# Kernel optimization log

Measured on AMD Instinct MI355X. Metric: run time of the kernel, lower is better.

The kernel has to match this reference:

```python
import jax, jax.numpy as jnp
import numpy as np

N_NODES = 50000
N_EDGES = 600000
N_GRAPHS = 64
D_IN = 128
D_HID = 128
D_OUT = 64


def setup_inputs() -> dict:
    key = jax.random.key(0)
    ks = jax.random.split(key, 8)
    x = jax.random.normal(ks[0], (N_NODES, D_IN), dtype=jnp.float32)
    edge_index = jax.random.randint(ks[1], (2, N_EDGES), 0, N_NODES, dtype=jnp.int64)
    batch = jnp.sort(jax.random.randint(ks[2], (N_NODES,), 0, N_GRAPHS, dtype=jnp.int64))
    def glorot(k, fan_in, fan_out):
        s = jnp.sqrt(6.0 / (fan_in + fan_out))
        return jax.random.uniform(k, (fan_in, fan_out), jnp.float32, -s, s)
    return {
        "x": x, "edge_index": edge_index, "batch": batch,
        "W1": glorot(ks[3], D_IN, D_HID), "b1": jnp.zeros((D_HID,), jnp.float32),
        "W2": glorot(ks[4], D_HID, D_HID), "b2": jnp.zeros((D_HID,), jnp.float32),
        "W3": glorot(ks[5], D_HID, D_HID), "b3": jnp.zeros((D_HID,), jnp.float32),
        "W4": glorot(ks[6], D_HID, D_OUT), "b4": jnp.zeros((D_OUT,), jnp.float32),
    }


def _gcn_conv(x, W, b, src, dst, deg_inv_sqrt, n_nodes):
    # PyG GCNConv: h = x W; out_i = sum_{j->i} norm_ij h_j  (+ self loop) + b
    h = x @ W  # [N, F]
    norm = deg_inv_sqrt[src] * deg_inv_sqrt[dst]  # [E]
    agg = jax.ops.segment_sum(h[src] * norm[:, None], dst, num_segments=n_nodes)
    # self-loop contribution: norm_ii = deg_inv_sqrt[i]^2
    agg = agg + h * (deg_inv_sqrt * deg_inv_sqrt)[:, None]
    return agg + b


def reference(x, edge_index, batch, W1, b1, W2, b2, W3, b3, W4, b4):
    n = x.shape[0]
    src, dst = edge_index[0], edge_index[1]
    # degree including self loops (PyG add_self_loops + deg over dst)
    deg = jax.ops.segment_sum(jnp.ones_like(dst, dtype=x.dtype), dst, num_segments=n) + 1.0
    deg_inv_sqrt = jax.lax.rsqrt(deg)

    h = jax.nn.relu(_gcn_conv(x, W1, b1, src, dst, deg_inv_sqrt, n))
    h = jax.nn.relu(_gcn_conv(h, W2, b2, src, dst, deg_inv_sqrt, n))
    h = jax.nn.relu(_gcn_conv(h, W3, b3, src, dst, deg_inv_sqrt, n))
    h = _gcn_conv(h, W4, b4, src, dst, deg_inv_sqrt, n)

    # global mean pool over graphs in the batch
    sums = jax.ops.segment_sum(h, batch, num_segments=N_GRAPHS)  # [G, D_OUT]
    cnts = jax.ops.segment_sum(jnp.ones((n,), h.dtype), batch, num_segments=N_GRAPHS)
    hg = sums / jnp.maximum(cnts, 1.0)[:, None]
    return jnp.squeeze(hg)
```

## Files before the change

kernel.cpp:

```cpp
#include <hip/hip_runtime.h>
#include <hip/hip_bf16.h>

#define N_NODES 50000
#define N_EDGES 600000
#define N_GRAPHS 64
#define PCHUNK 16

typedef __attribute__((ext_vector_type(8))) short bf16x8;
typedef __attribute__((ext_vector_type(4))) float f32x4;

__device__ __forceinline__ unsigned short f2bf(float f) {
    unsigned int u = __float_as_uint(f);
    unsigned int r = u + 0x7fffu + ((u >> 16) & 1u);
    return (unsigned short)(r >> 16);
}
__device__ __forceinline__ float bf_lo(unsigned int u) { return __uint_as_float(u << 16); }
__device__ __forceinline__ float bf_hi(unsigned int u) { return __uint_as_float(u & 0xffff0000u); }
__device__ __forceinline__ float bf1(unsigned short s) {
    return __uint_as_float((unsigned int)s << 16);
}

__device__ __forceinline__ void wprep_one(const float* W, unsigned short* Wp, int F, int idx) {
    int i = idx & 7;
    int lane = (idx >> 3) & 63;
    int ks = (idx >> 9) & 3;
    int ct = idx >> 11;
    int k = ks * 32 + (lane >> 4) * 8 + i;
    int col = ct * 16 + (lane & 15);
    Wp[idx] = f2bf(W[(size_t)k * F + col]);
}

__global__ __launch_bounds__(256) void deg_wprep(const int* __restrict__ dst,
                                                 int* __restrict__ degi, int E,
                                                 const float* __restrict__ W1,
                                                 const float* __restrict__ W2,
                                                 const float* __restrict__ W3,
                                                 const float* __restrict__ W4,
                                                 unsigned short* __restrict__ Wp1,
                                                 unsigned short* __restrict__ Wp2,
                                                 unsigned short* __restrict__ Wp3,
                                                 unsigned short* __restrict__ Wp4) {
    const int DEGB = (N_EDGES + 255) / 256;
    int bid = blockIdx.x;
    if (bid < DEGB) {
        int i = bid * 256 + threadIdx.x;
        if (i < E) atomicAdd(&degi[dst[i]], 1);
    } else {
        int wb = bid - DEGB;
        if (wb < 64) wprep_one(W1, Wp1, 128, wb * 256 + threadIdx.x);
        else if (wb < 128) wprep_one(W2, Wp2, 128, (wb - 64) * 256 + threadIdx.x);
        else if (wb < 192) wprep_one(W3, Wp3, 128, (wb - 128) * 256 + threadIdx.x);
        else wprep_one(W4, Wp4, 64, (wb - 192) * 256 + threadIdx.x);
    }
}

__global__ __launch_bounds__(256) void scan_block(const int* __restrict__ in,
                                                  int* __restrict__ excl,
                                                  int* __restrict__ bsum,
                                                  float* __restrict__ dis, int N) {
    __shared__ int s[256];
    int i = blockIdx.x * 256 + threadIdx.x;
    int v = (i < N) ? in[i] : 0;
    s[threadIdx.x] = v;
    __syncthreads();
#pragma unroll
    for (int off = 1; off < 256; off <<= 1) {
        int t = (threadIdx.x >= off) ? s[threadIdx.x - off] : 0;
        __syncthreads();
        s[threadIdx.x] += t;
        __syncthreads();
    }
    if (i < N) {
        excl[i] = s[threadIdx.x] - v;
        dis[i] = rsqrtf((float)v + 1.0f);
    }
    if (threadIdx.x == 255) bsum[blockIdx.x] = s[255];
}

__global__ __launch_bounds__(256) void scan_top(const int* __restrict__ bsum,
                                                int* __restrict__ boff, int NB,
                                                const int* __restrict__ batch,
                                                int* __restrict__ gstart, int N) {
    __shared__ int s[256];
    int v = (threadIdx.x < NB) ? bsum[threadIdx.x] : 0;
    s[threadIdx.x] = v;
    __syncthreads();
#pragma unroll
    for (int off = 1; off < 256; off <<= 1) {
        int t = (threadIdx.x >= off) ? s[threadIdx.x - off] : 0;
        __syncthreads();
        s[threadIdx.x] += t;
        __syncthreads();
    }
    if (threadIdx.x < NB) boff[threadIdx.x] = s[threadIdx.x] - v;

    int g = threadIdx.x;
    if (g <= N_GRAPHS) {
        int lo = 0, hi = N;
        while (lo < hi) {
            int mid = (lo + hi) >> 1;
            if (batch[mid] < g) lo = mid + 1; else hi = mid;
        }
        gstart[g] = lo;
    }
}

__global__ __launch_bounds__(256) void scan_fix(const int* __restrict__ excl,
                                                const int* __restrict__ boff,
                                                int* __restrict__ rowptr,
                                                int* __restrict__ cursor, int N, int E) {
    int i = blockIdx.x * 256 + threadIdx.x;
    if (i < N) {
        int r = excl[i] + boff[blockIdx.x];
        rowptr[i] = r;
        cursor[i] = r;
    }
    if (i == 0) rowptr[N] = E;
}

__global__ __launch_bounds__(256) void csr_fill(const int* __restrict__ src,
                                                const int* __restrict__ dst,
                                                const float* __restrict__ dis,
                                                int* __restrict__ cursor,
                                                int2* __restrict__ csr, int E) {
    int e = blockIdx.x * blockDim.x + threadIdx.x;
    if (e >= E) return;
    int s = src[e];
    int d = dst[e];
    float nrm = dis[s] * dis[d];
    int pos = atomicAdd(&cursor[d], 1);
    csr[pos] = make_int2(s, __float_as_int(nrm));
}

__device__ __forceinline__ void gather128(int beg, int end, const int2* __restrict__ csr,
                                          const unsigned short* __restrict__ T, int lane,
                                          float& ax, float& ay) {
    int p = beg;
    for (; p + 8 <= end; p += 8) {
        int2 e0 = csr[p], e1 = csr[p + 1], e2 = csr[p + 2], e3 = csr[p + 3];
        int2 e4 = csr[p + 4], e5 = csr[p + 5], e6 = csr[p + 6], e7 = csr[p + 7];
        unsigned int r0 = *reinterpret_cast<const unsigned int*>(T + (size_t)e0.x * 128 + lane * 2);
        unsigned int r1 = *reinterpret_cast<const unsigned int*>(T + (size_t)e1.x * 128 + lane * 2);
        unsigned int r2 = *reinterpret_cast<const unsigned int*>(T + (size_t)e2.x * 128 + lane * 2);
        unsigned int r3 = *reinterpret_cast<const unsigned int*>(T + (size_t)e3.x * 128 + lane * 2);
        unsigned int r4 = *reinterpret_cast<const unsigned int*>(T + (size_t)e4.x * 128 + lane * 2);
        unsigned int r5 = *reinterpret_cast<const unsigned int*>(T + (size_t)e5.x * 128 + lane * 2);
        unsigned int r6 = *reinterpret_cast<const unsigned int*>(T + (size_t)e6.x * 128 + lane * 2);
        unsigned int r7 = *reinterpret_cast<const unsigned int*>(T + (size_t)e7.x * 128 + lane * 2);
        float n0 = __int_as_float(e0.y), n1 = __int_as_float(e1.y);
        float n2 = __int_as_float(e2.y), n3 = __int_as_float(e3.y);
        float n4 = __int_as_float(e4.y), n5 = __int_as_float(e5.y);
        float n6 = __int_as_float(e6.y), n7 = __int_as_float(e7.y);
        ax = fmaf(n0, bf_lo(r0), ax); ay = fmaf(n0, bf_hi(r0), ay);
        ax = fmaf(n1, bf_lo(r1), ax); ay = fmaf(n1, bf_hi(r1), ay);
        ax = fmaf(n2, bf_lo(r2), ax); ay = fmaf(n2, bf_hi(r2), ay);
        ax = fmaf(n3, bf_lo(r3), ax); ay = fmaf(n3, bf_hi(r3), ay);
        ax = fmaf(n4, bf_lo(r4), ax); ay = fmaf(n4, bf_hi(r4), ay);
        ax = fmaf(n5, bf_lo(r5), ax); ay = fmaf(n5, bf_hi(r5), ay);
        ax = fmaf(n6, bf_lo(r6), ax); ay = fmaf(n6, bf_hi(r6), ay);
        ax = fmaf(n7, bf_lo(r7), ax); ay = fmaf(n7, bf_hi(r7), ay);
    }
    for (; p + 4 <= end; p += 4) {
        int2 e0 = csr[p], e1 = csr[p + 1], e2 = csr[p + 2], e3 = csr[p + 3];
        unsigned int r0 = *reinterpret_cast<const unsigned int*>(T + (size_t)e0.x * 128 + lane * 2);
        unsigned int r1 = *reinterpret_cast<const unsigned int*>(T + (size_t)e1.x * 128 + lane * 2);
        unsigned int r2 = *reinterpret_cast<const unsigned int*>(T + (size_t)e2.x * 128 + lane * 2);
        unsigned int r3 = *reinterpret_cast<const unsigned int*>(T + (size_t)e3.x * 128 + lane * 2);
        float n0 = __int_as_float(e0.y), n1 = __int_as_float(e1.y);
        float n2 = __int_as_float(e2.y), n3 = __int_as_float(e3.y);
        ax = fmaf(n0, bf_lo(r0), ax); ay = fmaf(n0, bf_hi(r0), ay);
        ax = fmaf(n1, bf_lo(r1), ax); ay = fmaf(n1, bf_hi(r1), ay);
        ax = fmaf(n2, bf_lo(r2), ax); ay = fmaf(n2, bf_hi(r2), ay);
        ax = fmaf(n3, bf_lo(r3), ax); ay = fmaf(n3, bf_hi(r3), ay);
    }
    for (; p < end; ++p) {
        int2 ed = csr[p];
        float nrm = __int_as_float(ed.y);
        unsigned int r = *reinterpret_cast<const unsigned int*>(T + (size_t)ed.x * 128 + lane * 2);
        ax = fmaf(nrm, bf_lo(r), ax);
        ay = fmaf(nrm, bf_hi(r), ay);
    }
}

__global__ __launch_bounds__(256) void mm_mfma1(const float* __restrict__ Xf,
                                                const unsigned short* __restrict__ Wp,
                                                unsigned short* __restrict__ T, int N) {
    const int lane = threadIdx.x & 63;
    const int wave = threadIdx.x >> 6;
    const int r0 = blockIdx.x * 64 + wave * 16;
    const int kg = lane >> 4;
    const int rdrow = min(r0 + (lane & 15), N - 1);
    const float* xr = Xf + (size_t)rdrow * 128;

    bf16x8 a[4];
#pragma unroll
    for (int ks = 0; ks < 4; ++ks) {
        const int kb = ks * 32 + kg * 8;
        float4 x0 = *reinterpret_cast<const float4*>(xr + kb);
        float4 x1 = *reinterpret_cast<const float4*>(xr + kb + 4);
        float v[8] = {x0.x, x0.y, x0.z, x0.w, x1.x, x1.y, x1.z, x1.w};
#pragma unroll
        for (int i = 0; i < 8; ++i) a[ks][i] = (short)f2bf(v[i]);
    }

#pragma unroll
    for (int ct = 0; ct < 8; ++ct) {
        f32x4 acc = {0.f, 0.f, 0.f, 0.f};
#pragma unroll
        for (int ks = 0; ks < 4; ++ks) {
            bf16x8 b = *reinterpret_cast<const bf16x8*>(Wp + ((size_t)(ct * 4 + ks) * 64 + lane) * 8);
            acc = __builtin_amdgcn_mfma_f32_16x16x32_bf16(a[ks], b, acc, 0, 0, 0);
        }
        const int col = ct * 16 + (lane & 15);
#pragma unroll
        for (int r = 0; r < 4; ++r) {
            const int rowm = r0 + kg * 4 + r;
            if (rowm < N) T[(size_t)rowm * 128 + col] = f2bf(acc[r]);
        }
    }
}

template <int FOUT>
__global__ __launch_bounds__(512) void aggmm(const int* __restrict__ rowptr,
                                             const int2* __restrict__ csr,
                                             const float* __restrict__ dis,
                                             const float* __restrict__ b,
                                             const unsigned short* __restrict__ T,
                                             const unsigned short* __restrict__ Wp,
                                             unsigned short* __restrict__ Tout, int N) {
    __shared__ unsigned short hl[16][136];
    const int lane = threadIdx.x & 63;
    const int wave = threadIdx.x >> 6;
    const int r0 = blockIdx.x * 16;
    const float2 bb = *reinterpret_cast<const float2*>(b + lane * 2);

#pragma unroll 1
    for (int i = 0; i < 2; ++i) {
        const int row = wave * 2 + i;
        const int node = __builtin_amdgcn_readfirstlane(r0 + row);
        if (node >= N) {
            *reinterpret_cast<unsigned int*>(&hl[row][lane * 2]) = 0u;
            continue;
        }
        const int beg = rowptr[node];
        const int end = rowptr[node + 1];
        const float d = dis[node];
        const float d2 = d * d;
        unsigned int selfv =
            *reinterpret_cast<const unsigned int*>(T + (size_t)node * 128 + lane * 2);
        float ax = fmaf(bf_lo(selfv), d2, bb.x);
        float ay = fmaf(bf_hi(selfv), d2, bb.y);
        gather128(beg, end, csr, T, lane, ax, ay);
        unsigned int packed = ((unsigned int)f2bf(ay) << 16) | (unsigned int)f2bf(ax);
        *reinterpret_cast<unsigned int*>(&hl[row][lane * 2]) = packed;
    }
    __syncthreads();

    constexpr int NCT = FOUT / 16;
    if (wave < NCT) {
        const int kg = lane >> 4;
        bf16x8 a[4];
#pragma unroll
        for (int ks = 0; ks < 4; ++ks) {
            bf16x8 av = *reinterpret_cast<const bf16x8*>(&hl[lane & 15][ks * 32 + kg * 8]);
#pragma unroll
            for (int i = 0; i < 8; ++i) av[i] = (av[i] < 0) ? (short)0 : av[i];
            a[ks] = av;
        }

        const int ct = wave;
        f32x4 acc = {0.f, 0.f, 0.f, 0.f};
#pragma unroll
        for (int ks = 0; ks < 4; ++ks) {
            bf16x8 bfr = *reinterpret_cast<const bf16x8*>(Wp + ((size_t)(ct * 4 + ks) * 64 + lane) * 8);
            acc = __builtin_amdgcn_mfma_f32_16x16x32_bf16(a[ks], bfr, acc, 0, 0, 0);
        }
        const int col = ct * 16 + (lane & 15);
#pragma unroll
        for (int r = 0; r < 4; ++r) {
            const int rowm = r0 + kg * 4 + r;
            if (rowm < N) Tout[(size_t)rowm * FOUT + col] = f2bf(acc[r]);
        }
    }
}

__global__ __launch_bounds__(256) void agg64(const int* __restrict__ rowptr,
                                             const int2* __restrict__ csr,
                                             const float* __restrict__ dis,
                                             const float* __restrict__ b,
                                             const unsigned short* __restrict__ T,
                                             unsigned short* __restrict__ H, int N) {
    const int lane = threadIdx.x & 63;
    const int node = __builtin_amdgcn_readfirstlane((blockIdx.x * 256 + threadIdx.x) >> 6);
    if (node >= N) return;

    const int beg = rowptr[node];
    const int end = rowptr[node + 1];
    const float d = dis[node];
    const float d2 = d * d;
    float a = fmaf(bf1(T[(size_t)node * 64 + lane]), d2, b[lane]);

    int p = beg;
    for (; p + 8 <= end; p += 8) {
        int2 e0 = csr[p], e1 = csr[p + 1], e2 = csr[p + 2], e3 = csr[p + 3];
        int2 e4 = csr[p + 4], e5 = csr[p + 5], e6 = csr[p + 6], e7 = csr[p + 7];
        unsigned short v0 = T[(size_t)e0.x * 64 + lane];
        unsigned short v1 = T[(size_t)e1.x * 64 + lane];
        unsigned short v2 = T[(size_t)e2.x * 64 + lane];
        unsigned short v3 = T[(size_t)e3.x * 64 + lane];
        unsigned short v4 = T[(size_t)e4.x * 64 + lane];
        unsigned short v5 = T[(size_t)e5.x * 64 + lane];
        unsigned short v6 = T[(size_t)e6.x * 64 + lane];
        unsigned short v7 = T[(size_t)e7.x * 64 + lane];
        a = fmaf(__int_as_float(e0.y), bf1(v0), a);
        a = fmaf(__int_as_float(e1.y), bf1(v1), a);
        a = fmaf(__int_as_float(e2.y), bf1(v2), a);
        a = fmaf(__int_as_float(e3.y), bf1(v3), a);
        a = fmaf(__int_as_float(e4.y), bf1(v4), a);
        a = fmaf(__int_as_float(e5.y), bf1(v5), a);
        a = fmaf(__int_as_float(e6.y), bf1(v6), a);
        a = fmaf(__int_as_float(e7.y), bf1(v7), a);
    }
    for (; p + 4 <= end; p += 4) {
        int2 e0 = csr[p], e1 = csr[p + 1], e2 = csr[p + 2], e3 = csr[p + 3];
        unsigned short v0 = T[(size_t)e0.x * 64 + lane];
        unsigned short v1 = T[(size_t)e1.x * 64 + lane];
        unsigned short v2 = T[(size_t)e2.x * 64 + lane];
        unsigned short v3 = T[(size_t)e3.x * 64 + lane];
        a = fmaf(__int_as_float(e0.y), bf1(v0), a);
        a = fmaf(__int_as_float(e1.y), bf1(v1), a);
        a = fmaf(__int_as_float(e2.y), bf1(v2), a);
        a = fmaf(__int_as_float(e3.y), bf1(v3), a);
    }
    for (; p < end; ++p) {
        int2 ed = csr[p];
        a = fmaf(__int_as_float(ed.y), bf1(T[(size_t)ed.x * 64 + lane]), a);
    }
    H[(size_t)node * 64 + lane] = f2bf(a);
}

__global__ __launch_bounds__(256) void pool_partial(const unsigned short* __restrict__ H,
                                                    const int* __restrict__ gstart,
                                                    float* __restrict__ partial) {
    const int g = blockIdx.x >> 4;
    const int c = blockIdx.x & (PCHUNK - 1);
    const int beg = gstart[g], end = gstart[g + 1];
    const int len = end - beg;
    const int csz = (len + PCHUNK - 1) / PCHUNK;
    const int cb = beg + c * csz;
    const int ce = min(cb + csz, end);
    const int lane = threadIdx.x & 63;
    const int wave = threadIdx.x >> 6;

    float acc = 0.0f;
    for (int n = cb + wave; n < ce; n += 4)
        acc += bf1(H[(size_t)n * 64 + lane]);

    __shared__ float s[4][64];
    s[wave][lane] = acc;
    __syncthreads();
    if (wave == 0)
        partial[(size_t)(g * PCHUNK + c) * 64 + lane] =
            s[0][lane] + s[1][lane] + s[2][lane] + s[3][lane];
}

__global__ __launch_bounds__(64) void pool_fin(const float* __restrict__ partial,
                                               const int* __restrict__ gstart,
                                               float* __restrict__ out) {
    const int g = blockIdx.x;
    const int lane = threadIdx.x;
    float v = 0.0f;
#pragma unroll
    for (int c = 0; c < PCHUNK; ++c) v += partial[(size_t)(g * PCHUNK + c) * 64 + lane];
    float cnt = (float)(gstart[g + 1] - gstart[g]);
    out[g * 64 + lane] = v / fmaxf(cnt, 1.0f);
}

extern "C" void kernel_launch(void* const* d_in, const int* in_sizes, int n_in,
                              void* d_out, int out_size, void* d_ws, size_t ws_size,
                              hipStream_t stream) {
    const float* x = (const float*)d_in[0];
    const int* ei = (const int*)d_in[1];
    const int* batch = (const int*)d_in[2];
    const float* W1 = (const float*)d_in[3];
    const float* b1 = (const float*)d_in[4];
    const float* W2 = (const float*)d_in[5];
    const float* b2 = (const float*)d_in[6];
    const float* W3 = (const float*)d_in[7];
    const float* b3 = (const float*)d_in[8];
    const float* W4 = (const float*)d_in[9];
    const float* b4 = (const float*)d_in[10];

    const int N = N_NODES, E = N_EDGES;
    const int* src = ei;
    const int* dst = ei + E;

    char* base = (char*)d_ws;
    size_t off = 0;
    auto carve = [&](size_t bytes) -> void* {
        off = (off + 63) & ~(size_t)63;
        void* p = base + off;
        off += bytes;
        return p;
    };
    unsigned short* Ta = (unsigned short*)carve((size_t)N * 128 * 2);
    unsigned short* Tb = (unsigned short*)carve((size_t)N * 128 * 2);
    unsigned short* H = (unsigned short*)carve((size_t)N * 64 * 2);
    int* degi = (int*)carve((size_t)N * 4);
    float* dis = (float*)carve((size_t)N * 4);
    int* rowptr = (int*)carve((size_t)(N + 1) * 4);
    int* cursor = (int*)carve((size_t)N * 4);
    int* excl = (int*)carve((size_t)N * 4);
    int* bsum = (int*)carve(256 * 4);
    int* boff = (int*)carve(256 * 4);
    int2* csr = (int2*)carve((size_t)E * 8);
    int* gstart = (int*)carve(65 * 4);
    float* partial = (float*)carve((size_t)N_GRAPHS * PCHUNK * 64 * 4);
    unsigned short* Wp1 = (unsigned short*)carve(128 * 128 * 2);
    unsigned short* Wp2 = (unsigned short*)carve(128 * 128 * 2);
    unsigned short* Wp3 = (unsigned short*)carve(128 * 128 * 2);
    unsigned short* Wp4 = (unsigned short*)carve(128 * 64 * 2);

    hipMemsetAsync(degi, 0, N * sizeof(int), stream);

    const int NB = (N + 255) / 256;
    const int DEGB = (E + 255) / 256;
    deg_wprep<<<DEGB + 224, 256, 0, stream>>>(dst, degi, E, W1, W2, W3, W4,
                                              Wp1, Wp2, Wp3, Wp4);
    scan_block<<<NB, 256, 0, stream>>>(degi, excl, bsum, dis, N);
    scan_top<<<1, 256, 0, stream>>>(bsum, boff, NB, batch, gstart, N);
    scan_fix<<<NB, 256, 0, stream>>>(excl, boff, rowptr, cursor, N, E);
    csr_fill<<<(E + 255) / 256, 256, 0, stream>>>(src, dst, dis, cursor, csr, E);

    const int MMG = (N + 63) / 64;
    const int FUS = (N + 15) / 16;

    mm_mfma1<<<MMG, 256, 0, stream>>>(x, Wp1, Ta, N);
    aggmm<128><<<FUS, 512, 0, stream>>>(rowptr, csr, dis, b1, Ta, Wp2, Tb, N);
    aggmm<128><<<FUS, 512, 0, stream>>>(rowptr, csr, dis, b2, Tb, Wp3, Ta, N);
    aggmm<64><<<FUS, 512, 0, stream>>>(rowptr, csr, dis, b3, Ta, Wp4, Tb, N);
    agg64<<<(N * 64 + 255) / 256, 256, 0, stream>>>(rowptr, csr, dis, b4, Tb, H, N);

    pool_partial<<<N_GRAPHS * PCHUNK, 256, 0, stream>>>(H, gstart, partial);
    pool_fin<<<N_GRAPHS, 64, 0, stream>>>(partial, gstart, (float*)d_out);
}
```

Baseline: 207.1 us.

## Pack CSR entries to 32-bit, merge scans, fuse CSR fill with first matmul

Each CSR edge entry is packed into one 32-bit word, holding a 16-bit source index and an fp16 normalization factor, which halves the edge-list traffic in every aggregation pass. The three-kernel prefix scan becomes a single 1024-thread block that also computes dis and gstart. The CSR fill and the first MFMA matmul now run as one launch, cutting the kernel count and letting the two overlap. The risks are that source indices must fit in 16 bits (N_NODES is 50000, so they do) and that storing the norm in fp16 loses precision. The single-block scan also runs serially over about 49 elements per thread.

Result: slower. 329.2 us (+59.0%).

```diff
diff --git a/kernel.cpp b/kernel.cpp
--- a/kernel.cpp
+++ b/kernel.cpp
@@ -1,10 +1,13 @@
 #include <hip/hip_runtime.h>
 #include <hip/hip_bf16.h>
+#include <hip/hip_fp16.h>
 
 #define N_NODES 50000
 #define N_EDGES 600000
 #define N_GRAPHS 64
 #define PCHUNK 16
+#define SCAN_T 1024
+#define SCAN_C ((N_NODES + SCAN_T - 1) / SCAN_T)
 
 typedef __attribute__((ext_vector_type(8))) short bf16x8;
 typedef __attribute__((ext_vector_type(4))) float f32x4;
@@ -18,6 +21,9 @@
 __device__ __forceinline__ float bf_hi(unsigned int u) { return __uint_as_float(u & 0xffff0000u); }
 __device__ __forceinline__ float bf1(unsigned short s) {
     return __uint_as_float((unsigned int)s << 16);
+}
+__device__ __forceinline__ float pnorm(unsigned int e) {
+    return __half2float(__ushort_as_half((unsigned short)(e & 0xffffu)));
 }
 
 __device__ __forceinline__ void wprep_one(const float* W, unsigned short* Wp, int F, int idx) {
@@ -54,103 +60,130 @@
     }
 }
 
-__global__ __launch_bounds__(256) void scan_block(const int* __restrict__ in,
-                                                  int* __restrict__ excl,
-                                                  int* __restrict__ bsum,
-                                                  float* __restrict__ dis, int N) {
-    __shared__ int s[256];
-    int i = blockIdx.x * 256 + threadIdx.x;
-    int v = (i < N) ? in[i] : 0;
-    s[threadIdx.x] = v;
+__global__ __launch_bounds__(SCAN_T) void scan_all(const int* __restrict__ degi,
+                                                   int* __restrict__ rowptr,
+                                                   int* __restrict__ cursor,
+                                                   float* __restrict__ dis,
+                                                   const int* __restrict__ batch,
+                                                   int* __restrict__ gstart) {
+    __shared__ int s[SCAN_T];
+    const int t = threadIdx.x;
+    const int c0 = t * SCAN_C;
+
+    int sum = 0;
+#pragma unroll 1
+    for (int j = 0; j < SCAN_C; ++j) {
+        int i = c0 + j;
+        if (i < N_NODES) sum += degi[i];
+    }
+    s[t] = sum;
     __syncthreads();
 #pragma unroll
-    for (int off = 1; off < 256; off <<= 1) {
-        int t = (threadIdx.x >= off) ? s[threadIdx.x - off] : 0;
+    for (int off = 1; off < SCAN_T; off <<= 1) {
+        int v = (t >= off) ? s[t - off] : 0;
         __syncthreads();
-        s[threadIdx.x] += t;
+        s[t] += v;
         __syncthreads();
     }
-    if (i < N) {
-        excl[i] = s[threadIdx.x] - v;
-        dis[i] = rsqrtf((float)v + 1.0f);
-    }
-    if (threadIdx.x == 255) bsum[blockIdx.x] = s[255];
-}
-
-__global__ __launch_bounds__(256) void scan_top(const int* __restrict__ bsum,
-                                                int* __restrict__ boff, int NB,
-                                                const int* __restrict__ batch,
-                                                int* __restrict__ gstart, int N) {
-    __shared__ int s[256];
-    int v = (threadIdx.x < NB) ? bsum[threadIdx.x] : 0;
-    s[threadIdx.x] = v;
-    __syncthreads();
-#pragma unroll
-    for (int off = 1; off < 256; off <<= 1) {
-        int t = (threadIdx.x >= off) ? s[threadIdx.x - off] : 0;
-        __syncthreads();
-        s[threadIdx.x] += t;
-        __syncthreads();
-    }
-    if (threadIdx.x < NB) boff[threadIdx.x] = s[threadIdx.x] - v;
-
-    int g = threadIdx.x;
-    if (g <= N_GRAPHS) {
-        int lo = 0, hi = N;
+    int base = s[t] - sum;
+
+#pragma unroll 1
+    for (int j = 0; j < SCAN_C; ++j) {
+        int i = c0 + j;
+        if (i < N_NODES) {
+            int d = degi[i];
+            rowptr[i] = base;
+            cursor[i] = base;
+            dis[i] = rsqrtf((float)d + 1.0f);
+            base += d;
+        }
+    }
+    if (t == 0) rowptr[N_NODES] = N_EDGES;
+
+    if (t <= N_GRAPHS) {
+        int lo = 0, hi = N_NODES;
         while (lo < hi) {
             int mid = (lo + hi) >> 1;
-            if (batch[mid] < g) lo = mid + 1; else hi = mid;
-        }
-        gstart[g] = lo;
-    }
-}
-
-__global__ __launch_bounds__(256) void scan_fix(const int* __restrict__ excl,
-                                                const int* __restrict__ boff,
-                                                int* __restrict__ rowptr,
-                                                int* __restrict__ cursor, int N, int E) {
-    int i = blockIdx.x * 256 + threadIdx.x;
-    if (i < N) {
-        int r = excl[i] + boff[blockIdx.x];
-        rowptr[i] = r;
-        cursor[i] = r;
-    }
-    if (i == 0) rowptr[N] = E;
-}
-
-__global__ __launch_bounds__(256) void csr_fill(const int* __restrict__ src,
-                                                const int* __restrict__ dst,
-                                                const float* __restrict__ dis,
-                                                int* __restrict__ cursor,
-                                                int2* __restrict__ csr, int E) {
-    int e = blockIdx.x * blockDim.x + threadIdx.x;
-    if (e >= E) return;
-    int s = src[e];
-    int d = dst[e];
-    float nrm = dis[s] * dis[d];
-    int pos = atomicAdd(&cursor[d], 1);
-    csr[pos] = make_int2(s, __float_as_int(nrm));
-}
-
-__device__ __forceinline__ void gather128(int beg, int end, const int2* __restrict__ csr,
+            if (batch[mid] < t) lo = mid + 1; else hi = mid;
+        }
+        gstart[t] = lo;
+    }
+}
+
+#define MM1B ((N_NODES + 63) / 64)
+#define CSRB ((N_EDGES + 255) / 256)
+
+__global__ __launch_bounds__(256) void csrfill_mm1(const int* __restrict__ src,
+                                                   const int* __restrict__ dst,
+                                                   const float* __restrict__ dis,
+                                                   int* __restrict__ cursor,
+                                                   unsigned int* __restrict__ csr, int E,
+                                                   const float* __restrict__ Xf,
+                                                   const unsigned short* __restrict__ Wp,
+                                                   unsigned short* __restrict__ T, int N) {
+    if (blockIdx.x >= MM1B) {
+        int e = (blockIdx.x - MM1B) * 256 + threadIdx.x;
+        if (e >= E) return;
+        int s = src[e];
+        int d = dst[e];
+        float nrm = dis[s] * dis[d];
+        unsigned short hb = __half_as_ushort(__float2half(nrm));
+        int pos = atomicAdd(&cursor[d], 1);
+        csr[pos] = ((unsigned int)s << 16) | (unsigned int)hb;
+        return;
+    }
+    const int lane = threadIdx.x & 63;
+    const int wave = threadIdx.x >> 6;
+    const int r0 = blockIdx.x * 64 + wave * 16;
+    const int kg = lane >> 4;
+    const int rdrow = min(r0 + (lane & 15), N - 1);
+    const float* xr = Xf + (size_t)rdrow * 128;
+
+    bf16x8 a[4];
+#pragma unroll
+    for (int ks = 0; ks < 4; ++ks) {
+        const int kb = ks * 32 + kg * 8;
+        float4 x0 = *reinterpret_cast<const float4*>(xr + kb);
+        float4 x1 = *reinterpret_cast<const float4*>(xr + kb + 4);
+        float v[8] = {x0.x, x0.y, x0.z, x0.w, x1.x, x1.y, x1.z, x1.w};
+#pragma unroll
+        for (int i = 0; i < 8; ++i) a[ks][i] = (short)f2bf(v[i]);
+    }
+
+#pragma unroll
+    for (int ct = 0; ct < 8; ++ct) {
+        f32x4 acc = {0.f, 0.f, 0.f, 0.f};
+#pragma unroll
+        for (int ks = 0; ks < 4; ++ks) {
+            bf16x8 b = *reinterpret_cast<const bf16x8*>(Wp + ((size_t)(ct * 4 + ks) * 64 + lane) * 8);
+            acc = __builtin_amdgcn_mfma_f32_16x16x32_bf16(a[ks], b, acc, 0, 0, 0);
+        }
+        const int col = ct * 16 + (lane & 15);
+#pragma unroll
+        for (int r = 0; r < 4; ++r) {
+            const int rowm = r0 + kg * 4 + r;
+            if (rowm < N) T[(size_t)rowm * 128 + col] = f2bf(acc[r]);
+        }
+    }
+}
+
+__device__ __forceinline__ void gather128(int beg, int end, const unsigned int* __restrict__ csr,
                                           const unsigned short* __restrict__ T, int lane,
                                           float& ax, float& ay) {
     int p = beg;
     for (; p + 8 <= end; p += 8) {
-        int2 e0 = csr[p], e1 = csr[p + 1], e2 = csr[p + 2], e3 = csr[p + 3];
-        int2 e4 = csr[p + 4], e5 = csr[p + 5], e6 = csr[p + 6], e7 = csr[p + 7];
-        unsigned int r0 = *reinterpret_cast<const unsigned int*>(T + (size_t)e0.x * 128 + lane * 2);
-        unsigned int r1 = *reinterpret_cast<const unsigned int*>(T + (size_t)e1.x * 128 + lane * 2);
-        unsigned int r2 = *reinterpret_cast<const unsigned int*>(T + (size_t)e2.x * 128 + lane * 2);
-        unsigned int r3 = *reinterpret_cast<const unsigned int*>(T + (size_t)e3.x * 128 + lane * 2);
-        unsigned int r4 = *reinterpret_cast<const unsigned int*>(T + (size_t)e4.x * 128 + lane * 2);
-        unsigned int r5 = *reinterpret_cast<const unsigned int*>(T + (size_t)e5.x * 128 + lane * 2);
-        unsigned int r6 = *reinterpret_cast<const unsigned int*>(T + (size_t)e6.x * 128 + lane * 2);
-        unsigned int r7 = *reinterpret_cast<const unsigned int*>(T + (size_t)e7.x * 128 + lane * 2);
-        float n0 = __int_as_float(e0.y), n1 = __int_as_float(e1.y);
-        float n2 = __int_as_float(e2.y), n3 = __int_as_float(e3.y);
-        float n4 = __int_as_float(e4.y), n5 = __int_as_float(e5.y);
-        float n6 = __int_as_float(e6.y), n7 = __int_as_float(e7.y);
+        unsigned int e0 = csr[p], e1 = csr[p + 1], e2 = csr[p + 2], e3 = csr[p + 3];
+        unsigned int e4 = csr[p + 4], e5 = csr[p + 5], e6 = csr[p + 6], e7 = csr[p + 7];
+        unsigned int r0 = *reinterpret_cast<const unsigned int*>(T + (size_t)(e0 >> 16) * 128 + lane * 2);
+        unsigned int r1 = *reinterpret_cast<const unsigned int*>(T + (size_t)(e1 >> 16) * 128 + lane * 2);
+        unsigned int r2 = *reinterpret_cast<const unsigned int*>(T + (size_t)(e2 >> 16) * 128 + lane * 2);
+        unsigned int r3 = *reinterpret_cast<const unsigned int*>(T + (size_t)(e3 >> 16) * 128 + lane * 2);
+        unsigned int r4 = *reinterpret_cast<const unsigned int*>(T + (size_t)(e4 >> 16) * 128 + lane * 2);
+        unsigned int r5 = *reinterpret_cast<const unsigned int*>(T + (size_t)(e5 >> 16) * 128 + lane * 2);
+        unsigned int r6 = *reinterpret_cast<const unsigned int*>(T + (size_t)(e6 >> 16) * 128 + lane * 2);
+        unsigned int r7 = *reinterpret_cast<const unsigned int*>(T + (size_t)(e7 >> 16) * 128 + lane * 2);
+        float n0 = pnorm(e0), n1 = pnorm(e1), n2 = pnorm(e2), n3 = pnorm(e3);
+        float n4 = pnorm(e4), n5 = pnorm(e5), n6 = pnorm(e6), n7 = pnorm(e7);
         ax = fmaf(n0, bf_lo(r0), ax); ay = fmaf(n0, bf_hi(r0), ay);
         ax = fmaf(n1, bf_lo(r1), ax); ay = fmaf(n1, bf_hi(r1), ay);
         ax = fmaf(n2, bf_lo(r2), ax); ay = fmaf(n2, bf_hi(r2), ay);
@@ -161,68 +194,29 @@
         ax = fmaf(n7, bf_lo(r7), ax); ay = fmaf(n7, bf_hi(r7), ay);
     }
     for (; p + 4 <= end; p += 4) {
-        int2 e0 = csr[p], e1 = csr[p + 1], e2 = csr[p + 2], e3 = csr[p + 3];
-        unsigned int r0 = *reinterpret_cast<const unsigned int*>(T + (size_t)e0.x * 128 + lane * 2);
-        unsigned int r1 = *reinterpret_cast<const unsigned int*>(T + (size_t)e1.x * 128 + lane * 2);
-        unsigned int r2 = *reinterpret_cast<const unsigned int*>(T + (size_t)e2.x * 128 + lane * 2);
-        unsigned int r3 = *reinterpret_cast<const unsigned int*>(T + (size_t)e3.x * 128 + lane * 2);
-        float n0 = __int_as_float(e0.y), n1 = __int_as_float(e1.y);
-        float n2 = __int_as_float(e2.y), n3 = __int_as_float(e3.y);
+        unsigned int e0 = csr[p], e1 = csr[p + 1], e2 = csr[p + 2], e3 = csr[p + 3];
+        unsigned int r0 = *reinterpret_cast<const unsigned int*>(T + (size_t)(e0 >> 16) * 128 + lane * 2);
+        unsigned int r1 = *reinterpret_cast<const unsigned int*>(T + (size_t)(e1 >> 16) * 128 + lane * 2);
+        unsigned int r2 = *reinterpret_cast<const unsigned int*>(T + (size_t)(e2 >> 16) * 128 + lane * 2);
+        unsigned int r3 = *reinterpret_cast<const unsigned int*>(T + (size_t)(e3 >> 16) * 128 + lane * 2);
+        float n0 = pnorm(e0), n1 = pnorm(e1), n2 = pnorm(e2), n3 = pnorm(e3);
         ax = fmaf(n0, bf_lo(r0), ax); ay = fmaf(n0, bf_hi(r0), ay);
         ax = fmaf(n1, bf_lo(r1), ax); ay = fmaf(n1, bf_hi(r1), ay);
         ax = fmaf(n2, bf_lo(r2), ax); ay = fmaf(n2, bf_hi(r2), ay);
         ax = fmaf(n3, bf_lo(r3), ax); ay = fmaf(n3, bf_hi(r3), ay);
     }
     for (; p < end; ++p) {
-        int2 ed = csr[p];
-        float nrm = __int_as_float(ed.y);
-        unsigned int r = *reinterpret_cast<const unsigned int*>(T + (size_t)ed.x * 128 + lane * 2);
+        unsigned int e = csr[p];
+        float nrm = pnorm(e);
+        unsigned int r = *reinterpret_cast<const unsigned int*>(T + (size_t)(e >> 16) * 128 + lane * 2);
         ax = fmaf(nrm, bf_lo(r), ax);
         ay = fmaf(nrm, bf_hi(r), ay);
     }
 }
 
-__global__ __launch_bounds__(256) void mm_mfma1(const float* __restrict__ Xf,
-                                                const unsigned short* __restrict__ Wp,
-                                                unsigned short* __restrict__ T, int N) {
-    const int lane = threadIdx.x & 63;
-    const int wave = threadIdx.x >> 6;
-    const int r0 = blockIdx.x * 64 + wave * 16;
-    const int kg = lane >> 4;
-    const int rdrow = min(r0 + (lane & 15), N - 1);
-    const float* xr = Xf + (size_t)rdrow * 128;
-
-    bf16x8 a[4];
-#pragma unroll
-    for (int ks = 0; ks < 4; ++ks) {
-        const int kb = ks * 32 + kg * 8;
-        float4 x0 = *reinterpret_cast<const float4*>(xr + kb);
-        float4 x1 = *reinterpret_cast<const float4*>(xr + kb + 4);
-        float v[8] = {x0.x, x0.y, x0.z, x0.w, x1.x, x1.y, x1.z, x1.w};
-#pragma unroll
-        for (int i = 0; i < 8; ++i) a[ks][i] = (short)f2bf(v[i]);
-    }
-
-#pragma unroll
-    for (int ct = 0; ct < 8; ++ct) {
-        f32x4 acc = {0.f, 0.f, 0.f, 0.f};
-#pragma unroll
-        for (int ks = 0; ks < 4; ++ks) {
-            bf16x8 b = *reinterpret_cast<const bf16x8*>(Wp + ((size_t)(ct * 4 + ks) * 64 + lane) * 8);
-            acc = __builtin_amdgcn_mfma_f32_16x16x32_bf16(a[ks], b, acc, 0, 0, 0);
-        }
-        const int col = ct * 16 + (lane & 15);
-#pragma unroll
-        for (int r = 0; r < 4; ++r) {
-            const int rowm = r0 + kg * 4 + r;
-            if (rowm < N) T[(size_t)rowm * 128 + col] = f2bf(acc[r]);
-        }
-    }
-}
-
 template <int FOUT>
 __global__ __launch_bounds__(512) void aggmm(const int* __restrict__ rowptr,
-                                             const int2* __restrict__ csr,
+                                             const unsigned int* __restrict__ csr,
                                              const float* __restrict__ dis,
                                              const float* __restrict__ b,
                                              const unsigned short* __restrict__ T,
@@ -285,7 +279,7 @@
 }
 
 __global__ __launch_bounds__(256) void agg64(const int* __restrict__ rowptr,
-                                             const int2* __restrict__ csr,
+                                             const unsigned int* __restrict__ csr,
                                              const float* __restrict__ dis,
                                              const float* __restrict__ b,
                                              const unsigned short* __restrict__ T,
@@ -302,39 +296,39 @@
 
     int p = beg;
     for (; p + 8 <= end; p += 8) {
-        int2 e0 = csr[p], e1 = csr[p + 1], e2 = csr[p + 2], e3 = csr[p + 3];
-        int2 e4 = csr[p + 4], e5 = csr[p + 5], e6 = csr[p + 6], e7 = csr[p + 7];
-        unsigned short v0 = T[(size_t)e0.x * 64 + lane];
-        unsigned short v1 = T[(size_t)e1.x * 64 + lane];
-        unsigned short v2 = T[(size_t)e2.x * 64 + lane];
-        unsigned short v3 = T[(size_t)e3.x * 64 + lane];
-        unsigned short v4 = T[(size_t)e4.x * 64 + lane];
-        unsigned short v5 = T[(size_t)e5.x * 64 + lane];
-        unsigned short v6 = T[(size_t)e6.x * 64 + lane];
-        unsigned short v7 = T[(size_t)e7.x * 64 + lane];
-        a = fmaf(__int_as_float(e0.y), bf1(v0), a);
-        a = fmaf(__int_as_float(e1.y), bf1(v1), a);
-        a = fmaf(__int_as_float(e2.y), bf1(v2), a);
-        a = fmaf(__int_as_float(e3.y), bf1(v3), a);
-        a = fmaf(__int_as_float(e4.y), bf1(v4), a);
-        a = fmaf(__int_as_float(e5.y), bf1(v5), a);
-        a = fmaf(__int_as_float(e6.y), bf1(v6), a);
-        a = fmaf(__int_as_float(e7.y), bf1(v7), a);
+        unsigned int e0 = csr[p], e1 = csr[p + 1], e2 = csr[p + 2], e3 = csr[p + 3];
+        unsigned int e4 = csr[p + 4], e5 = csr[p + 5], e6 = csr[p + 6], e7 = csr[p + 7];
+        unsigned short v0 = T[(size_t)(e0 >> 16) * 64 + lane];
+        unsigned short v1 = T[(size_t)(e1 >> 16) * 64 + lane];
+        unsigned short v2 = T[(size_t)(e2 >> 16) * 64 + lane];
+        unsigned short v3 = T[(size_t)(e3 >> 16) * 64 + lane];
+        unsigned short v4 = T[(size_t)(e4 >> 16) * 64 + lane];
+        unsigned short v5 = T[(size_t)(e5 >> 16) * 64 + lane];
+        unsigned short v6 = T[(size_t)(e6 >> 16) * 64 + lane];
+        unsigned short v7 = T[(size_t)(e7 >> 16) * 64 + lane];
+        a = fmaf(pnorm(e0), bf1(v0), a);
+        a = fmaf(pnorm(e1), bf1(v1), a);
+        a = fmaf(pnorm(e2), bf1(v2), a);
+        a = fmaf(pnorm(e3), bf1(v3), a);
+        a = fmaf(pnorm(e4), bf1(v4), a);
+        a = fmaf(pnorm(e5), bf1(v5), a);
+        a = fmaf(pnorm(e6), bf1(v6), a);
+        a = fmaf(pnorm(e7), bf1(v7), a);
     }
     for (; p + 4 <= end; p += 4) {
-        int2 e0 = csr[p], e1 = csr[p + 1], e2 = csr[p + 2], e3 = csr[p + 3];
-        unsigned short v0 = T[(size_t)e0.x * 64 + lane];
-        unsigned short v1 = T[(size_t)e1.x * 64 + lane];
-        unsigned short v2 = T[(size_t)e2.x * 64 + lane];
-        unsigned short v3 = T[(size_t)e3.x * 64 + lane];
-        a = fmaf(__int_as_float(e0.y), bf1(v0), a);
-        a = fmaf(__int_as_float(e1.y), bf1(v1), a);
-        a = fmaf(__int_as_float(e2.y), bf1(v2), a);
-        a = fmaf(__int_as_float(e3.y), bf1(v3), a);
+        unsigned int e0 = csr[p], e1 = csr[p + 1], e2 = csr[p + 2], e3 = csr[p + 3];
+        unsigned short v0 = T[(size_t)(e0 >> 16) * 64 + lane];
+        unsigned short v1 = T[(size_t)(e1 >> 16) * 64 + lane];
+        unsigned short v2 = T[(size_t)(e2 >> 16) * 64 + lane];
+        unsigned short v3 = T[(size_t)(e3 >> 16) * 64 + lane];
+        a = fmaf(pnorm(e0), bf1(v0), a);
+        a = fmaf(pnorm(e1), bf1(v1), a);
+        a = fmaf(pnorm(e2), bf1(v2), a);
+        a = fmaf(pnorm(e3), bf1(v3), a);
     }
     for (; p < end; ++p) {
-        int2 ed = csr[p];
-        a = fmaf(__int_as_float(ed.y), bf1(T[(size_t)ed.x * 64 + lane]), a);
+        unsigned int e = csr[p];
+        a = fmaf(pnorm(e), bf1(T[(size_t)(e >> 16) * 64 + lane]), a);
     }
     H[(size_t)node * 64 + lane] = f2bf(a);
 }
@@ -410,10 +404,7 @@
     float* dis = (float*)carve((size_t)N * 4);
     int* rowptr = (int*)carve((size_t)(N + 1) * 4);
     int* cursor = (int*)carve((size_t)N * 4);
-    int* excl = (int*)carve((size_t)N * 4);
-    int* bsum = (int*)carve(256 * 4);
-    int* boff = (int*)carve(256 * 4);
-    int2* csr = (int2*)carve((size_t)E * 8);
+    unsigned int* csr = (unsigned int*)carve((size_t)E * 4);
     int* gstart = (int*)carve(65 * 4);
     float* partial = (float*)carve((size_t)N_GRAPHS * PCHUNK * 64 * 4);
     unsigned short* Wp1 = (unsigned short*)carve(128 * 128 * 2);
@@ -423,19 +414,15 @@
 
     hipMemsetAsync(degi, 0, N * sizeof(int), stream);
 
-    const int NB = (N + 255) / 256;
     const int DEGB = (E + 255) / 256;
     deg_wprep<<<DEGB + 224, 256, 0, stream>>>(dst, degi, E, W1, W2, W3, W4,
                                               Wp1, Wp2, Wp3, Wp4);
-    scan_block<<<NB, 256, 0, stream>>>(degi, excl, bsum, dis, N);
-    scan_top<<<1, 256, 0, stream>>>(bsum, boff, NB, batch, gstart, N);
-    scan_fix<<<NB, 256, 0, stream>>>(excl, boff, rowptr, cursor, N, E);
-    csr_fill<<<(E + 255) / 256, 256, 0, stream>>>(src, dst, dis, cursor, csr, E);
-
-    const int MMG = (N + 63) / 64;
+    scan_all<<<1, SCAN_T, 0, stream>>>(degi, rowptr, cursor, dis, batch, gstart);
+    csrfill_mm1<<<MM1B + CSRB, 256, 0, stream>>>(src, dst, dis, cursor, csr, E,
+                                                 x, Wp1, Ta, N);
+
     const int FUS = (N + 15) / 16;
 
-    mm_mfma1<<<MMG, 256, 0, stream>>>(x, Wp1, Ta, N);
     aggmm<128><<<FUS, 512, 0, stream>>>(rowptr, csr, dis, b1, Ta, Wp2, Tb, N);
     aggmm<128><<<FUS, 512, 0, stream>>>(rowptr, csr, dis, b2, Tb, Wp3, Ta, N);
     aggmm<64><<<FUS, 512, 0, stream>>>(rowptr, csr, dis, b3, Ta, Wp4, Tb, N);
```
